# Kernel tuning notes

Measured on AMD Instinct MI355X. Metric: run time of the kernel, lower is better.

The kernel has to match this reference:

```python
import jax, jax.numpy as jnp
import numpy as np

ROPE_BASE = 10000.0
NEG_INF = jnp.finfo(jnp.float32).min


def _rope_tables(T, head_dim):
    inv_freq = 1.0 / (ROPE_BASE ** (jnp.arange(0, head_dim, 2, dtype=jnp.float32) / head_dim))
    t = jnp.arange(T, dtype=jnp.float32)
    freqs = jnp.einsum('i,j->ij', t, inv_freq)          # [T, head_dim/2]
    emb = jnp.concatenate([freqs, freqs], axis=-1)      # [T, head_dim]
    return jnp.cos(emb), jnp.sin(emb)


def _rotate_half(x):
    d = x.shape[-1] // 2
    return jnp.concatenate([-x[..., d:], x[..., :d]], axis=-1)


def setup_inputs() -> dict:
    key = jax.random.key(0)
    ks = jax.random.split(key, 6)
    B, T, C = 2, 2048, 1024
    s = 0.02
    return {
        'x': jax.random.normal(ks[0], (B, T, C), jnp.float32),
        'attn_mask': jnp.ones((B, T), jnp.int32),
        'wq': jax.random.normal(ks[1], (C, C), jnp.float32) * s,
        'wk': jax.random.normal(ks[2], (C, C), jnp.float32) * s,
        'wv': jax.random.normal(ks[3], (C, C), jnp.float32) * s,
        'wo': jax.random.normal(ks[4], (C, C), jnp.float32) * s,
        'bo': jnp.zeros((C,), jnp.float32),
        'is_causal': 1,
    }


def reference(x, attn_mask, wq, wk, wv, wo, bo, is_causal):
    B, T, C = x.shape
    H = 16
    D = C // H

    q = (x @ wq).reshape(B, T, H, D).transpose(0, 2, 1, 3)  # [B,H,T,D]
    k = (x @ wk).reshape(B, T, H, D).transpose(0, 2, 1, 3)
    v = (x @ wv).reshape(B, T, H, D).transpose(0, 2, 1, 3)

    # inline RoPE (self-attention path); note scaling_factor = 1.0 in this branch,
    # faithful to the original module.
    cos, sin = _rope_tables(T, D)            # [T, D]
    cos = cos[None, None]                    # [1,1,T,D]
    sin = sin[None, None]
    q = q * cos + _rotate_half(q) * sin
    k = k * cos + _rotate_half(k) * sin

    scores = jnp.einsum('bhqd,bhkd->bhqk', q, k)  # [B,H,T,T], scale 1.0 w/ RoPE

    # mask union: padding mask (2D attn_mask) OR causal mask
    pad_mask = ~(attn_mask.astype(bool))[:, None, None, :]            # [B,1,1,T]
    causal = jnp.triu(jnp.ones((T, T), bool), k=1)[None, None]        # [1,1,T,T]
    if is_causal:
        final_mask = pad_mask | causal
    else:
        final_mask = pad_mask
    scores = jnp.where(final_mask, NEG_INF, scores)

    attn = jax.nn.softmax(scores, axis=-1)   # dropout omitted (eval mode)
    out = jnp.einsum('bhqk,bhkd->bhqd', attn, v)
    out = out.transpose(0, 2, 1, 3).reshape(B, T, C)
    return out @ wo + bo
```

## Files before the change

kernel.cpp:

```cpp
#include <hip/hip_runtime.h>
#include <hip/hip_bf16.h>
#include <stdint.h>

#define B_ 2
#define T_ 2048
#define C_ 1024
#define H_ 16
#define D_ 64
#define NEG_INF_F (-3.4028234663852886e38f)

typedef __bf16 bf16;
typedef __bf16 bf16x4 __attribute__((ext_vector_type(4)));
typedef __bf16 bf16x8 __attribute__((ext_vector_type(8)));
typedef float  f32x4  __attribute__((ext_vector_type(4)));

__device__ __forceinline__ void gload16(const bf16* g, bf16* l) {
  __builtin_amdgcn_global_load_lds(
      (const __attribute__((address_space(1))) void*)(g),
      (__attribute__((address_space(3))) void*)(l), 16, 0, 0);
}

__device__ __forceinline__ f32x4 mfma16(bf16x8 a, bf16x8 b, f32x4 c) {
  return __builtin_amdgcn_mfma_f32_16x16x32_bf16(a, b, c, 0, 0, 0);
}


__global__ void k_prep_x(const float* __restrict__ x, bf16* __restrict__ xb) {
  int i = (blockIdx.x * 256 + threadIdx.x) * 4;
  float4 v = *(const float4*)(x + i);
  bf16x4 o;
  o[0] = (bf16)v.x; o[1] = (bf16)v.y; o[2] = (bf16)v.z; o[3] = (bf16)v.w;
  *(bf16x4*)(xb + i) = o;
}

__global__ void k_rope(float* __restrict__ rc, float* __restrict__ rs) {
  int i = blockIdx.x * 256 + threadIdx.x;
  int t = i >> 5, d = i & 31;
  float inv = expf(-(float)(2 * d) * (9.210340371976184f / 64.0f));
  float fr = (float)t * inv;
  rc[i] = cosf(fr);
  rs[i] = sinf(fr);
}

__global__ void k_maskprep(const int* __restrict__ amask, float* __restrict__ negm,
                           unsigned char* __restrict__ tileclean) {
  int b = blockIdx.x;
  int tid = threadIdx.x;
  int base = b * T_ + tid * 8;
  int4 a0 = *(const int4*)(amask + base);
  int4 a1 = *(const int4*)(amask + base + 4);
  bool ok = a0.x && a0.y && a0.z && a0.w && a1.x && a1.y && a1.z && a1.w;
  float4 f0, f1;
  f0.x = a0.x ? 0.f : NEG_INF_F; f0.y = a0.y ? 0.f : NEG_INF_F;
  f0.z = a0.z ? 0.f : NEG_INF_F; f0.w = a0.w ? 0.f : NEG_INF_F;
  f1.x = a1.x ? 0.f : NEG_INF_F; f1.y = a1.y ? 0.f : NEG_INF_F;
  f1.z = a1.z ? 0.f : NEG_INF_F; f1.w = a1.w ? 0.f : NEG_INF_F;
  *(float4*)(negm + base) = f0;
  *(float4*)(negm + base + 4) = f1;
  unsigned long long m = __ballot(ok);
  int w = tid >> 6, lane = tid & 63;
  if (lane < 8) {
    tileclean[b * 32 + w * 8 + lane] =
        (unsigned char)(((m >> (lane * 8)) & 0xFFull) == 0xFFull);
  }
}

__global__ void k_prep_w(const float* __restrict__ wq, const float* __restrict__ wk,
                         const float* __restrict__ wv, const float* __restrict__ wo,
                         bf16* __restrict__ wqkvT, bf16* __restrict__ woT) {
  __shared__ float tile[32][33];
  int mat = blockIdx.z;
  const float* src = (mat == 0) ? wq : (mat == 1) ? wk : (mat == 2) ? wv : wo;
  bf16* dst = (mat < 3) ? (wqkvT + (size_t)mat * C_ * C_) : woT;
  int k0 = blockIdx.y * 32, n0 = blockIdx.x * 32;
  int tx = threadIdx.x & 31, ty = threadIdx.x >> 5;
  #pragma unroll
  for (int r = 0; r < 32; r += 8)
    tile[ty + r][tx] = src[(size_t)(k0 + ty + r) * C_ + n0 + tx];
  __syncthreads();
  #pragma unroll
  for (int r = 0; r < 32; r += 8)
    dst[(size_t)(n0 + ty + r) * C_ + k0 + tx] = (bf16)tile[tx][ty + r];
}

template <int MODE>
__global__ __launch_bounds__(256, 2)
void k_gemm(const bf16* __restrict__ A, const bf16* __restrict__ BT,
            const float* __restrict__ rc, const float* __restrict__ rs,
            bf16* __restrict__ qb, bf16* __restrict__ kbuf, bf16* __restrict__ vtb,
            const float* __restrict__ bo, float* __restrict__ outp) {
  constexpr int K = C_;
  __shared__ __align__(16) bf16 lA[128 * 32];
  __shared__ __align__(16) bf16 lB[128 * 32];
  const int tid = threadIdx.x;
  const int m0 = blockIdx.y * 128, n0 = blockIdx.x * 128;
  const int lane = tid & 63, w = tid >> 6;
  const int l15 = lane & 15, g = lane >> 4;
  const int wm = (w >> 1) * 64, wn = (w & 1) * 64;

  f32x4 acc[4][4] = {};

  const int srow = tid >> 2;
  const int skb = tid & 3;
  const int scol = ((skb ^ ((srow ^ (srow >> 2)) & 3)) << 3);
  const bf16* gA = A + (size_t)(m0 + srow) * K + scol;
  const bf16* gB = BT + (size_t)(n0 + srow) * K + scol;
  bf16* sA = lA + tid * 8;
  bf16* sB = lB + tid * 8;

  const int fsw = ((l15 ^ (l15 >> 2)) & 3);

  for (int k0 = 0; k0 < K; k0 += 32) {
    gload16(gA + k0, sA);
    gload16(gA + (size_t)64 * K + k0, sA + 2048);
    gload16(gB + k0, sB);
    gload16(gB + (size_t)64 * K + k0, sB + 2048);
    __syncthreads();

    bf16x8 af[4], bfr[4];
    #pragma unroll
    for (int i = 0; i < 4; i++) {
      int row = wm + i * 16 + l15;
      af[i] = *(const bf16x8*)(lA + row * 32 + ((g ^ fsw) << 3));
      int rowb = wn + i * 16 + l15;
      bfr[i] = *(const bf16x8*)(lB + rowb * 32 + ((g ^ fsw) << 3));
    }
    #pragma unroll
    for (int i = 0; i < 4; i++)
      #pragma unroll
      for (int j = 0; j < 4; j++)
        acc[i][j] = mfma16(af[i], bfr[j], acc[i][j]);
    __syncthreads();
  }

  if constexpr (MODE == 0) {
    const int region = n0 >> 10;
    const int nr = (n0 & 1023) + wn;
    const int h = nr >> 6;
    if (region < 2) {
      bf16* dst = (region == 0) ? qb : kbuf;
      #pragma unroll
      for (int i = 0; i < 4; i++) {
        #pragma unroll
        for (int r = 0; r < 4; r++) {
          int m = m0 + wm + i * 16 + g * 4 + r;
          int b = m >> 11, t = m & 2047;
          size_t base = ((size_t)(b * H_ + h) * T_ + t) * 64;
          #pragma unroll
          for (int j = 0; j < 2; j++) {
            int dl = j * 16 + l15;
            float c = rc[t * 32 + dl], s = rs[t * 32 + dl];
            float lo = acc[i][j][r], hi = acc[i][j + 2][r];
            dst[base + dl]      = (bf16)(lo * c - hi * s);
            dst[base + dl + 32] = (bf16)(hi * c + lo * s);
          }
        }
      }
    } else {
      #pragma unroll
      for (int i = 0; i < 4; i++)
        #pragma unroll
        for (int j = 0; j < 4; j++) {
          int d = j * 16 + l15;
          #pragma unroll
          for (int r = 0; r < 4; r++) {
            int m = m0 + wm + i * 16 + g * 4 + r;
            int b = m >> 11, t = m & 2047;
            vtb[((size_t)(b * H_ + h) * 64 + d) * T_ + t] = (bf16)acc[i][j][r];
          }
        }
    }
  } else {
    #pragma unroll
    for (int i = 0; i < 4; i++)
      #pragma unroll
      for (int j = 0; j < 4; j++) {
        int n = n0 + wn + j * 16 + l15;
        float bias = bo[n];
        #pragma unroll
        for (int r = 0; r < 4; r++) {
          int m = m0 + wm + i * 16 + g * 4 + r;
          outp[(size_t)m * C_ + n] = acc[i][j][r] + bias;
        }
      }
  }
}

__global__ __launch_bounds__(256, 4)
void k_attn(const bf16* __restrict__ qb, const bf16* __restrict__ kbuf,
            const bf16* __restrict__ vtb, const float* __restrict__ negm,
            const unsigned char* __restrict__ tileclean,
            const int* __restrict__ pcausal, bf16* __restrict__ ob) {
  __shared__ __align__(16) bf16 lK[64 * 64];
  __shared__ __align__(16) bf16 lV[64 * 64];
  __shared__ __align__(16) bf16 lP[4][16 * 64];
  const int bx = blockIdx.x;
  const int qi = 31 - (bx >> 5);
  const int bh = bx & 31;
  const int b = bh >> 4, h = bh & 15;
  const int causal = pcausal[0];
  const int tid = threadIdx.x, lane = tid & 63, w = tid >> 6;
  const int l15 = lane & 15, g = lane >> 4;
  const int sw7 = l15 & 7;
  const int q0 = qi * 64;
  const int wq0 = q0 + w * 16;
  const size_t plane = (size_t)(b * H_ + h) * T_ * 64;

  const int nkt = causal ? (qi + 1) : (T_ / 64);

  unsigned int bits = 0;
  {
    const unsigned char* tcb = tileclean + b * 32;
    #pragma unroll
    for (int i2 = 0; i2 < 32; i2++) bits |= ((unsigned int)tcb[i2]) << i2;
  }

  bf16x8 qf[2];
  #pragma unroll
  for (int kf = 0; kf < 2; kf++)
    qf[kf] = *(const bf16x8*)(qb + plane + (size_t)(wq0 + l15) * 64 + kf * 32 + g * 8);

  f32x4 o[4] = {};
  float psum[4] = {0.f, 0.f, 0.f, 0.f};

  const int srow = tid >> 3;
  const int skb = tid & 7;
  const int scol = ((skb ^ (srow & 7)) << 3);
  const bf16* gK = kbuf + plane + (size_t)srow * 64 + scol;
  const bf16* gV = vtb + plane + (size_t)srow * T_ + scol;
  bf16* sKd = lK + tid * 8;
  bf16* sVd = lV + tid * 8;
  bf16* myP = lP[w];

  for (int kt = 0; kt < nkt; kt++) {
    const size_t k0 = (size_t)kt * 64;
    gload16(gK + k0 * 64, sKd);
    gload16(gK + (k0 + 32) * 64, sKd + 2048);
    gload16(gV + k0, sVd);
    gload16(gV + (size_t)32 * T_ + k0, sVd + 2048);
    __syncthreads();

    f32x4 s[4] = {};
    #pragma unroll
    for (int j = 0; j < 4; j++) {
      const int kr = j * 16 + l15;
      bf16x8 k0f = *(const bf16x8*)(lK + kr * 64 + (((0 + g) ^ sw7) << 3));
      bf16x8 k1f = *(const bf16x8*)(lK + kr * 64 + (((4 + g) ^ sw7) << 3));
      s[j] = mfma16(qf[0], k0f, s[j]);
      s[j] = mfma16(qf[1], k1f, s[j]);
    }

    if (!((bits >> kt) & 1)) {
      #pragma unroll
      for (int j = 0; j < 4; j++) {
        float nm = negm[b * T_ + (int)k0 + j * 16 + l15];
        #pragma unroll
        for (int r = 0; r < 4; r++) s[j][r] += nm;
      }
    }
    if (causal && (kt == nkt - 1)) {
      #pragma unroll
      for (int j = 0; j < 4; j++) {
        const int kkg = (int)k0 + j * 16 + l15;
        #pragma unroll
        for (int r = 0; r < 4; r++) {
          const int qg = wq0 + g * 4 + r;
          if (kkg > qg) s[j][r] = NEG_INF_F;
        }
      }
    }

    #pragma unroll
    for (int r = 0; r < 4; r++) {
      float p0 = __expf(s[0][r]), p1 = __expf(s[1][r]);
      float p2 = __expf(s[2][r]), p3 = __expf(s[3][r]);
      s[0][r] = p0; s[1][r] = p1; s[2][r] = p2; s[3][r] = p3;
      psum[r] += (p0 + p1) + (p2 + p3);
    }

    #pragma unroll
    for (int j = 0; j < 4; j++) {
      const int col = j * 16 + l15;
      const int kb2 = col >> 3, c7 = col & 7;
      #pragma unroll
      for (int r = 0; r < 4; r++) {
        const int rw = g * 4 + r;
        myP[rw * 64 + ((kb2 ^ (rw & 7)) << 3) + c7] = (bf16)s[j][r];
      }
    }

    #pragma unroll
    for (int kt2 = 0; kt2 < 2; kt2++) {
      bf16x8 pa = *(const bf16x8*)(myP + l15 * 64 + (((kt2 * 4 + g) ^ sw7) << 3));
      #pragma unroll
      for (int df = 0; df < 4; df++) {
        bf16x8 bv = *(const bf16x8*)(lV + (df * 16 + l15) * 64 + (((kt2 * 4 + g) ^ sw7) << 3));
        o[df] = mfma16(pa, bv, o[df]);
      }
    }

    __syncthreads();
  }

  float inv[4];
  #pragma unroll
  for (int r = 0; r < 4; r++) {
    float t = psum[r];
    t += __shfl_xor(t, 1);
    t += __shfl_xor(t, 2);
    t += __shfl_xor(t, 4);
    t += __shfl_xor(t, 8);
    inv[r] = 1.0f / t;
  }
  #pragma unroll
  for (int df = 0; df < 4; df++) {
    const int d = df * 16 + l15;
    #pragma unroll
    for (int r = 0; r < 4; r++) {
      const int t = wq0 + g * 4 + r;
      ob[((size_t)(b * T_ + t)) * C_ + h * 64 + d] = (bf16)(o[df][r] * inv[r]);
    }
  }
}

extern "C" void kernel_launch(void* const* d_in, const int* in_sizes, int n_in,
                              void* d_out, int out_size, void* d_ws, size_t ws_size,
                              hipStream_t stream) {
  const float* x  = (const float*)d_in[0];
  const int* amask = (const int*)d_in[1];
  const float* wq = (const float*)d_in[2];
  const float* wk = (const float*)d_in[3];
  const float* wv = (const float*)d_in[4];
  const float* wo = (const float*)d_in[5];
  const float* bo = (const float*)d_in[6];
  const int* isc  = (const int*)d_in[7];
  float* outp = (float*)d_out;

  char* ws = (char*)d_ws;
  bf16* xb    = (bf16*)(ws);
  bf16* wqkvT = (bf16*)(ws + ((size_t)8 << 20));
  bf16* woT   = (bf16*)(ws + ((size_t)14 << 20));
  float* rc   = (float*)(ws + ((size_t)16 << 20));
  float* rs   = (float*)(ws + ((size_t)16 << 20) + (256 << 10));
  float* negm = (float*)(ws + ((size_t)16 << 20) + (512 << 10));
  unsigned char* tileclean = (unsigned char*)(ws + ((size_t)16 << 20) + (528 << 10));
  bf16* qbuf  = (bf16*)(ws + ((size_t)17 << 20));
  bf16* kbuf  = (bf16*)(ws + ((size_t)25 << 20));
  bf16* vtbuf = (bf16*)(ws + ((size_t)33 << 20));
  bf16* obuf  = (bf16*)(ws + ((size_t)41 << 20));

  hipLaunchKernelGGL(k_prep_x, dim3(4096), dim3(256), 0, stream, x, xb);
  hipLaunchKernelGGL(k_rope, dim3(256), dim3(256), 0, stream, rc, rs);
  hipLaunchKernelGGL(k_maskprep, dim3(B_), dim3(256), 0, stream, amask, negm, tileclean);
  hipLaunchKernelGGL(k_prep_w, dim3(32, 32, 4), dim3(256), 0, stream, wq, wk, wv, wo, wqkvT, woT);
  hipLaunchKernelGGL((k_gemm<0>), dim3(24, 32), dim3(256), 0, stream,
                     xb, wqkvT, rc, rs, qbuf, kbuf, vtbuf, nullptr, nullptr);
  hipLaunchKernelGGL(k_attn, dim3(1024), dim3(256), 0, stream,
                     qbuf, kbuf, vtbuf, negm, tileclean, isc, obuf);
  hipLaunchKernelGGL((k_gemm<1>), dim3(8, 32), dim3(256), 0, stream,
                     obuf, woT, nullptr, nullptr, nullptr, nullptr, nullptr, bo, outp);
}
```

Before: 196.2 us.

## Double-buffer attention K/V tiles, merge prep kernels, shrink output GEMM M-tile

The attention kernel now keeps two LDS buffers for K and V and issues the global-to-LDS loads for the next key tile before computing on the current one. The aim is to hide load latency behind the QK and PV MFMA work, at the cost of doubling K/V LDS use, which may limit occupancy. The RoPE-table, mask and weight-transpose prep kernels are merged into one launch to cut launch overhead. The output-projection GEMM gets a BM template parameter and runs with 64-row tiles, doubling its block count for better CU fill.

```diff
diff --git a/kernel.cpp b/kernel.cpp
--- a/kernel.cpp
+++ b/kernel.cpp
@@ -33,72 +33,76 @@
   *(bf16x4*)(xb + i) = o;
 }
 
-__global__ void k_rope(float* __restrict__ rc, float* __restrict__ rs) {
-  int i = blockIdx.x * 256 + threadIdx.x;
-  int t = i >> 5, d = i & 31;
-  float inv = expf(-(float)(2 * d) * (9.210340371976184f / 64.0f));
-  float fr = (float)t * inv;
-  rc[i] = cosf(fr);
-  rs[i] = sinf(fr);
-}
-
-__global__ void k_maskprep(const int* __restrict__ amask, float* __restrict__ negm,
+__global__ void k_prep_wrm(const float* __restrict__ wq, const float* __restrict__ wk,
+                           const float* __restrict__ wv, const float* __restrict__ wo,
+                           bf16* __restrict__ wqkvT, bf16* __restrict__ woT,
+                           float* __restrict__ rc, float* __restrict__ rs,
+                           const int* __restrict__ amask, float* __restrict__ negm,
                            unsigned char* __restrict__ tileclean) {
-  int b = blockIdx.x;
-  int tid = threadIdx.x;
-  int base = b * T_ + tid * 8;
-  int4 a0 = *(const int4*)(amask + base);
-  int4 a1 = *(const int4*)(amask + base + 4);
-  bool ok = a0.x && a0.y && a0.z && a0.w && a1.x && a1.y && a1.z && a1.w;
-  float4 f0, f1;
-  f0.x = a0.x ? 0.f : NEG_INF_F; f0.y = a0.y ? 0.f : NEG_INF_F;
-  f0.z = a0.z ? 0.f : NEG_INF_F; f0.w = a0.w ? 0.f : NEG_INF_F;
-  f1.x = a1.x ? 0.f : NEG_INF_F; f1.y = a1.y ? 0.f : NEG_INF_F;
-  f1.z = a1.z ? 0.f : NEG_INF_F; f1.w = a1.w ? 0.f : NEG_INF_F;
-  *(float4*)(negm + base) = f0;
-  *(float4*)(negm + base + 4) = f1;
-  unsigned long long m = __ballot(ok);
-  int w = tid >> 6, lane = tid & 63;
-  if (lane < 8) {
-    tileclean[b * 32 + w * 8 + lane] =
-        (unsigned char)(((m >> (lane * 8)) & 0xFFull) == 0xFFull);
-  }
-}
-
-__global__ void k_prep_w(const float* __restrict__ wq, const float* __restrict__ wk,
-                         const float* __restrict__ wv, const float* __restrict__ wo,
-                         bf16* __restrict__ wqkvT, bf16* __restrict__ woT) {
   __shared__ float tile[32][33];
-  int mat = blockIdx.z;
-  const float* src = (mat == 0) ? wq : (mat == 1) ? wk : (mat == 2) ? wv : wo;
-  bf16* dst = (mat < 3) ? (wqkvT + (size_t)mat * C_ * C_) : woT;
-  int k0 = blockIdx.y * 32, n0 = blockIdx.x * 32;
-  int tx = threadIdx.x & 31, ty = threadIdx.x >> 5;
-  #pragma unroll
-  for (int r = 0; r < 32; r += 8)
-    tile[ty + r][tx] = src[(size_t)(k0 + ty + r) * C_ + n0 + tx];
-  __syncthreads();
-  #pragma unroll
-  for (int r = 0; r < 32; r += 8)
-    dst[(size_t)(n0 + ty + r) * C_ + k0 + tx] = (bf16)tile[tx][ty + r];
-}
-
-template <int MODE>
+  const int mat = blockIdx.z;
+  const int tid = threadIdx.x;
+  if (mat < 4) {
+    const float* src = (mat == 0) ? wq : (mat == 1) ? wk : (mat == 2) ? wv : wo;
+    bf16* dst = (mat < 3) ? (wqkvT + (size_t)mat * C_ * C_) : woT;
+    int k0 = blockIdx.y * 32, n0 = blockIdx.x * 32;
+    int tx = tid & 31, ty = tid >> 5;
+    #pragma unroll
+    for (int r = 0; r < 32; r += 8)
+      tile[ty + r][tx] = src[(size_t)(k0 + ty + r) * C_ + n0 + tx];
+    __syncthreads();
+    #pragma unroll
+    for (int r = 0; r < 32; r += 8)
+      dst[(size_t)(n0 + ty + r) * C_ + k0 + tx] = (bf16)tile[tx][ty + r];
+    return;
+  }
+  const int flat = blockIdx.y * 32 + blockIdx.x;
+  if (flat < 256) {
+    int i = flat * 256 + tid;
+    int t = i >> 5, d = i & 31;
+    float inv = expf(-(float)(2 * d) * (9.210340371976184f / 64.0f));
+    float fr = (float)t * inv;
+    rc[i] = cosf(fr);
+    rs[i] = sinf(fr);
+  } else if (flat < 256 + B_) {
+    int b = flat - 256;
+    int base = b * T_ + tid * 8;
+    int4 a0 = *(const int4*)(amask + base);
+    int4 a1 = *(const int4*)(amask + base + 4);
+    bool ok = a0.x && a0.y && a0.z && a0.w && a1.x && a1.y && a1.z && a1.w;
+    float4 f0, f1;
+    f0.x = a0.x ? 0.f : NEG_INF_F; f0.y = a0.y ? 0.f : NEG_INF_F;
+    f0.z = a0.z ? 0.f : NEG_INF_F; f0.w = a0.w ? 0.f : NEG_INF_F;
+    f1.x = a1.x ? 0.f : NEG_INF_F; f1.y = a1.y ? 0.f : NEG_INF_F;
+    f1.z = a1.z ? 0.f : NEG_INF_F; f1.w = a1.w ? 0.f : NEG_INF_F;
+    *(float4*)(negm + base) = f0;
+    *(float4*)(negm + base + 4) = f1;
+    unsigned long long m = __ballot(ok);
+    int w = tid >> 6, lane = tid & 63;
+    if (lane < 8) {
+      tileclean[b * 32 + w * 8 + lane] =
+          (unsigned char)(((m >> (lane * 8)) & 0xFFull) == 0xFFull);
+    }
+  }
+}
+
+template <int MODE, int BM>
 __global__ __launch_bounds__(256, 2)
 void k_gemm(const bf16* __restrict__ A, const bf16* __restrict__ BT,
             const float* __restrict__ rc, const float* __restrict__ rs,
             bf16* __restrict__ qb, bf16* __restrict__ kbuf, bf16* __restrict__ vtb,
             const float* __restrict__ bo, float* __restrict__ outp) {
   constexpr int K = C_;
-  __shared__ __align__(16) bf16 lA[128 * 32];
+  constexpr int MI = BM / 32;
+  __shared__ __align__(16) bf16 lA[BM * 32];
   __shared__ __align__(16) bf16 lB[128 * 32];
   const int tid = threadIdx.x;
-  const int m0 = blockIdx.y * 128, n0 = blockIdx.x * 128;
+  const int m0 = blockIdx.y * BM, n0 = blockIdx.x * 128;
   const int lane = tid & 63, w = tid >> 6;
   const int l15 = lane & 15, g = lane >> 4;
-  const int wm = (w >> 1) * 64, wn = (w & 1) * 64;
-
-  f32x4 acc[4][4] = {};
+  const int wm = (w >> 1) * (BM / 2), wn = (w & 1) * 64;
+
+  f32x4 acc[MI][4] = {};
 
   const int srow = tid >> 2;
   const int skb = tid & 3;
@@ -112,21 +116,24 @@
 
   for (int k0 = 0; k0 < K; k0 += 32) {
     gload16(gA + k0, sA);
-    gload16(gA + (size_t)64 * K + k0, sA + 2048);
+    if constexpr (BM == 128) gload16(gA + (size_t)64 * K + k0, sA + 2048);
     gload16(gB + k0, sB);
     gload16(gB + (size_t)64 * K + k0, sB + 2048);
     __syncthreads();
 
-    bf16x8 af[4], bfr[4];
-    #pragma unroll
-    for (int i = 0; i < 4; i++) {
+    bf16x8 af[MI], bfr[4];
+    #pragma unroll
+    for (int i = 0; i < MI; i++) {
       int row = wm + i * 16 + l15;
       af[i] = *(const bf16x8*)(lA + row * 32 + ((g ^ fsw) << 3));
-      int rowb = wn + i * 16 + l15;
-      bfr[i] = *(const bf16x8*)(lB + rowb * 32 + ((g ^ fsw) << 3));
-    }
-    #pragma unroll
-    for (int i = 0; i < 4; i++)
+    }
+    #pragma unroll
+    for (int j = 0; j < 4; j++) {
+      int rowb = wn + j * 16 + l15;
+      bfr[j] = *(const bf16x8*)(lB + rowb * 32 + ((g ^ fsw) << 3));
+    }
+    #pragma unroll
+    for (int i = 0; i < MI; i++)
       #pragma unroll
       for (int j = 0; j < 4; j++)
         acc[i][j] = mfma16(af[i], bfr[j], acc[i][j]);
@@ -140,7 +147,7 @@
     if (region < 2) {
       bf16* dst = (region == 0) ? qb : kbuf;
       #pragma unroll
-      for (int i = 0; i < 4; i++) {
+      for (int i = 0; i < MI; i++) {
         #pragma unroll
         for (int r = 0; r < 4; r++) {
           int m = m0 + wm + i * 16 + g * 4 + r;
@@ -158,7 +165,7 @@
       }
     } else {
       #pragma unroll
-      for (int i = 0; i < 4; i++)
+      for (int i = 0; i < MI; i++)
         #pragma unroll
         for (int j = 0; j < 4; j++) {
           int d = j * 16 + l15;
@@ -172,7 +179,7 @@
     }
   } else {
     #pragma unroll
-    for (int i = 0; i < 4; i++)
+    for (int i = 0; i < MI; i++)
       #pragma unroll
       for (int j = 0; j < 4; j++) {
         int n = n0 + wn + j * 16 + l15;
@@ -191,8 +198,8 @@
             const bf16* __restrict__ vtb, const float* __restrict__ negm,
             const unsigned char* __restrict__ tileclean,
             const int* __restrict__ pcausal, bf16* __restrict__ ob) {
-  __shared__ __align__(16) bf16 lK[64 * 64];
-  __shared__ __align__(16) bf16 lV[64 * 64];
+  __shared__ __align__(16) bf16 lK[2][64 * 64];
+  __shared__ __align__(16) bf16 lV[2][64 * 64];
   __shared__ __align__(16) bf16 lP[4][16 * 64];
   const int bx = blockIdx.x;
   const int qi = 31 - (bx >> 5);
@@ -228,24 +235,41 @@
   const int scol = ((skb ^ (srow & 7)) << 3);
   const bf16* gK = kbuf + plane + (size_t)srow * 64 + scol;
   const bf16* gV = vtb + plane + (size_t)srow * T_ + scol;
-  bf16* sKd = lK + tid * 8;
-  bf16* sVd = lV + tid * 8;
   bf16* myP = lP[w];
 
+  {
+    bf16* sKd = lK[0] + tid * 8;
+    bf16* sVd = lV[0] + tid * 8;
+    gload16(gK, sKd);
+    gload16(gK + (size_t)32 * 64, sKd + 2048);
+    gload16(gV, sVd);
+    gload16(gV + (size_t)32 * T_, sVd + 2048);
+  }
+  __syncthreads();
+
+  int cur = 0;
   for (int kt = 0; kt < nkt; kt++) {
+    if (kt + 1 < nkt) {
+      const size_t nk0 = (size_t)(kt + 1) * 64;
+      bf16* sKd = lK[cur ^ 1] + tid * 8;
+      bf16* sVd = lV[cur ^ 1] + tid * 8;
+      gload16(gK + nk0 * 64, sKd);
+      gload16(gK + (nk0 + 32) * 64, sKd + 2048);
+      gload16(gV + nk0, sVd);
+      gload16(gV + (size_t)32 * T_ + nk0, sVd + 2048);
+    }
+    __builtin_amdgcn_sched_barrier(0);
+
+    const bf16* cK = lK[cur];
+    const bf16* cV = lV[cur];
     const size_t k0 = (size_t)kt * 64;
-    gload16(gK + k0 * 64, sKd);
-    gload16(gK + (k0 + 32) * 64, sKd + 2048);
-    gload16(gV + k0, sVd);
-    gload16(gV + (size_t)32 * T_ + k0, sVd + 2048);
-    __syncthreads();
 
     f32x4 s[4] = {};
     #pragma unroll
     for (int j = 0; j < 4; j++) {
       const int kr = j * 16 + l15;
-      bf16x8 k0f = *(const bf16x8*)(lK + kr * 64 + (((0 + g) ^ sw7) << 3));
-      bf16x8 k1f = *(const bf16x8*)(lK + kr * 64 + (((4 + g) ^ sw7) << 3));
+      bf16x8 k0f = *(const bf16x8*)(cK + kr * 64 + (((0 + g) ^ sw7) << 3));
+      bf16x8 k1f = *(const bf16x8*)(cK + kr * 64 + (((4 + g) ^ sw7) << 3));
       s[j] = mfma16(qf[0], k0f, s[j]);
       s[j] = mfma16(qf[1], k1f, s[j]);
     }
@@ -294,12 +318,13 @@
       bf16x8 pa = *(const bf16x8*)(myP + l15 * 64 + (((kt2 * 4 + g) ^ sw7) << 3));
       #pragma unroll
       for (int df = 0; df < 4; df++) {
-        bf16x8 bv = *(const bf16x8*)(lV + (df * 16 + l15) * 64 + (((kt2 * 4 + g) ^ sw7) << 3));
+        bf16x8 bv = *(const bf16x8*)(cV + (df * 16 + l15) * 64 + (((kt2 * 4 + g) ^ sw7) << 3));
         o[df] = mfma16(pa, bv, o[df]);
       }
     }
 
     __syncthreads();
+    cur ^= 1;
   }
 
   float inv[4];
@@ -350,13 +375,12 @@
   bf16* obuf  = (bf16*)(ws + ((size_t)41 << 20));
 
   hipLaunchKernelGGL(k_prep_x, dim3(4096), dim3(256), 0, stream, x, xb);
-  hipLaunchKernelGGL(k_rope, dim3(256), dim3(256), 0, stream, rc, rs);
-  hipLaunchKernelGGL(k_maskprep, dim3(B_), dim3(256), 0, stream, amask, negm, tileclean);
-  hipLaunchKernelGGL(k_prep_w, dim3(32, 32, 4), dim3(256), 0, stream, wq, wk, wv, wo, wqkvT, woT);
-  hipLaunchKernelGGL((k_gemm<0>), dim3(24, 32), dim3(256), 0, stream,
+  hipLaunchKernelGGL(k_prep_wrm, dim3(32, 32, 5), dim3(256), 0, stream,
+                     wq, wk, wv, wo, wqkvT, woT, rc, rs, amask, negm, tileclean);
+  hipLaunchKernelGGL((k_gemm<0, 128>), dim3(24, 32), dim3(256), 0, stream,
                      xb, wqkvT, rc, rs, qbuf, kbuf, vtbuf, nullptr, nullptr);
   hipLaunchKernelGGL(k_attn, dim3(1024), dim3(256), 0, stream,
                      qbuf, kbuf, vtbuf, negm, tileclean, isc, obuf);
-  hipLaunchKernelGGL((k_gemm<1>), dim3(8, 32), dim3(256), 0, stream,
+  hipLaunchKernelGGL((k_gemm<1, 64>), dim3(8, 64), dim3(256), 0, stream,
                      obuf, woT, nullptr, nullptr, nullptr, nullptr, nullptr, bo, outp);
 }
```

Measured after the change: 185.8 us. -5.3%, faster.
